# Kernel optimization log

Hardware: AMD Instinct MI355X
Metric: run time of the kernel (lower is better)

The kernel has to match this reference:

```python
import jax, jax.numpy as jnp
import numpy as np

N, K, D = 500000, 16, 16


def setup_inputs() -> dict:
    key = jax.random.key(0)
    k1, k2, k3, k4 = jax.random.split(key, 4)
    x = jax.random.normal(k1, (N, D), dtype=jnp.float32)
    # mixture weights: positive, sum to 1, shape (1, K)
    pi = jax.nn.softmax(jax.random.normal(k2, (1, K), dtype=jnp.float32), axis=-1)
    mu = jax.random.normal(k3, (K, 1, D), dtype=jnp.float32)
    # SPD covariance per cluster: A A^T / D + I
    A = jax.random.normal(k4, (K, D, D), dtype=jnp.float32)
    Sigma = jnp.einsum('kde,kfe->kdf', A, A) / D + jnp.eye(D, dtype=jnp.float32)
    return {"x": x, "pi": pi, "mu": mu, "Sigma": Sigma}


def reference(x, pi, mu, Sigma):
    # Batched MultivariateNormal log_prob over K clusters (replaces the
    # Python loop over torch.distributions.MultivariateNormal).
    d = x.shape[-1]
    L = jnp.linalg.cholesky(Sigma)                      # (K, D, D)
    diff = x[None, :, :] - mu                           # (K, N, D) via mu (K,1,D)
    # solve L y = diff^T per cluster -> Mahalanobis = ||y||^2
    y = jax.vmap(lambda Lk, dk: jax.scipy.linalg.solve_triangular(Lk, dk.T, lower=True))(L, diff)  # (K, D, N)
    maha = jnp.sum(y * y, axis=1)                       # (K, N)
    half_logdet = jnp.sum(jnp.log(jnp.diagonal(L, axis1=-2, axis2=-1)), axis=-1)  # (K,)
    log2pi = jnp.log(jnp.asarray(2.0 * np.pi, dtype=x.dtype))
    logp = -0.5 * (maha + d * log2pi) - half_logdet[:, None]  # (K, N)
    res_k = jnp.exp(logp).T * pi                        # (N, K), pi broadcasts from (1,K)
    res = res_k / jnp.sum(res_k, axis=1, keepdims=True)  # (N, K)
    return res
```

## Files before the change

### kernel.cpp

```cpp
#include <hip/hip_runtime.h>
#include <math.h>

#define D 16
#define K 16
#define BLK 64
#define MPT 2
#define PSTRIDE 176

__host__ __device__ constexpr int tri(int i, int j) { return i * (i + 1) / 2 + j; }

__global__ __launch_bounds__(64) void gmm_prep(
    const float* __restrict__ pi, const float* __restrict__ mu,
    const float* __restrict__ Sigma, float* __restrict__ P)
{
    const int k = threadIdx.x;
    if (k >= K) return;

    float M[tri(D - 1, D - 1) + 1];

#pragma unroll
    for (int i = 0; i < D; ++i)
#pragma unroll
        for (int j = 0; j <= i; ++j)
            M[tri(i, j)] = Sigma[k * D * D + i * D + j];

    float hl = 0.f;
#pragma unroll
    for (int j = 0; j < D; ++j) {
        float s = M[tri(j, j)];
#pragma unroll
        for (int p = 0; p < j; ++p) s -= M[tri(j, p)] * M[tri(j, p)];
        float ljj = sqrtf(s);
        M[tri(j, j)] = ljj;
        hl += logf(ljj);
        float inv = 1.f / ljj;
#pragma unroll
        for (int i = j + 1; i < D; ++i) {
            float t = M[tri(i, j)];
#pragma unroll
            for (int p = 0; p < j; ++p) t -= M[tri(i, p)] * M[tri(j, p)];
            M[tri(i, j)] = t * inv;
        }
    }

#pragma unroll
    for (int j = 0; j < D; ++j) {
        float ujj = 1.f / M[tri(j, j)];
        M[tri(j, j)] = ujj;
#pragma unroll
        for (int i = j + 1; i < D; ++i) {
            float s = 0.f;
#pragma unroll
            for (int p = j; p < i; ++p) s += M[tri(i, p)] * M[tri(p, j)];
            M[tri(i, j)] = -s / M[tri(i, i)];
        }
    }

    const float invs2 = 0.70710678118654752440f;
    float* Pk = P + k * PSTRIDE;
    Pk[0] = logf(pi[k]) - hl;
#pragma unroll
    for (int i = 0; i < D; ++i) {
        float acc = 0.f;
#pragma unroll
        for (int j = 0; j <= i; ++j) acc += M[tri(i, j)] * mu[k * D + j];
        Pk[16 + i] = acc * invs2;
    }
#pragma unroll
    for (int t = 0; t < tri(D - 1, D - 1) + 1; ++t)
        Pk[32 + t] = M[t] * invs2;
}

__global__ __launch_bounds__(BLK) void gmm_main(
    const float* __restrict__ x, const float* __restrict__ P,
    float* __restrict__ out, int N)
{
    const int tid = threadIdx.x;
    const long long base = (long long)blockIdx.x * (BLK * MPT) + tid;

    float xv[MPT][D];
    int   nidx[MPT];
    bool  ok[MPT];
#pragma unroll
    for (int m = 0; m < MPT; ++m) {
        long long n = base + (long long)m * BLK;
        nidx[m] = (int)n;
        ok[m] = (n < (long long)N);
        if (ok[m]) {
            const float4* p = (const float4*)(x + n * D);
            float4 a = p[0], b = p[1], c = p[2], d4 = p[3];
            xv[m][0] = a.x;  xv[m][1] = a.y;  xv[m][2] = a.z;  xv[m][3] = a.w;
            xv[m][4] = b.x;  xv[m][5] = b.y;  xv[m][6] = b.z;  xv[m][7] = b.w;
            xv[m][8] = c.x;  xv[m][9] = c.y;  xv[m][10] = c.z; xv[m][11] = c.w;
            xv[m][12] = d4.x; xv[m][13] = d4.y; xv[m][14] = d4.z; xv[m][15] = d4.w;
        } else {
#pragma unroll
            for (int j = 0; j < D; ++j) xv[m][j] = 0.f;
        }
    }

    float res[MPT][K];
#pragma unroll 1
    for (int k = 0; k < K; ++k) {
        const float* __restrict__ Pk = P + k * PSTRIDE;
        float acc[MPT];
#pragma unroll
        for (int m = 0; m < MPT; ++m) acc[m] = 0.f;
#pragma unroll
        for (int i = 0; i < D; ++i) {
            float tv = Pk[16 + i];
            float y[MPT];
#pragma unroll
            for (int m = 0; m < MPT; ++m) y[m] = -tv;
#pragma unroll
            for (int j = 0; j <= i; ++j) {
                float u = Pk[32 + tri(i, j)];
#pragma unroll
                for (int m = 0; m < MPT; ++m) y[m] = fmaf(u, xv[m][j], y[m]);
            }
#pragma unroll
            for (int m = 0; m < MPT; ++m) acc[m] = fmaf(y[m], y[m], acc[m]);
        }
        float ck = Pk[0];
#pragma unroll
        for (int m = 0; m < MPT; ++m) res[m][k] = ck - acc[m];
    }

#pragma unroll
    for (int m = 0; m < MPT; ++m) {
        if (!ok[m]) continue;
        float mx = res[m][0];
#pragma unroll
        for (int k2 = 1; k2 < K; ++k2) mx = fmaxf(mx, res[m][k2]);
        float sum = 0.f;
#pragma unroll
        for (int k2 = 0; k2 < K; ++k2) {
            float e = __expf(res[m][k2] - mx);
            res[m][k2] = e;
            sum += e;
        }
        float inv = 1.f / sum;
        float4* po = (float4*)(out + (long long)nidx[m] * K);
        float4 o;
        o.x = res[m][0] * inv;  o.y = res[m][1] * inv;
        o.z = res[m][2] * inv;  o.w = res[m][3] * inv;   po[0] = o;
        o.x = res[m][4] * inv;  o.y = res[m][5] * inv;
        o.z = res[m][6] * inv;  o.w = res[m][7] * inv;   po[1] = o;
        o.x = res[m][8] * inv;  o.y = res[m][9] * inv;
        o.z = res[m][10] * inv; o.w = res[m][11] * inv;  po[2] = o;
        o.x = res[m][12] * inv; o.y = res[m][13] * inv;
        o.z = res[m][14] * inv; o.w = res[m][15] * inv;  po[3] = o;
    }
}

extern "C" void kernel_launch(void* const* d_in, const int* in_sizes, int n_in,
                              void* d_out, int out_size, void* d_ws, size_t ws_size,
                              hipStream_t stream) {
    const float* x     = (const float*)d_in[0];
    const float* pi    = (const float*)d_in[1];
    const float* mu    = (const float*)d_in[2];
    const float* Sigma = (const float*)d_in[3];
    float* out = (float*)d_out;
    const int N = in_sizes[0] / D;

    float* P = (float*)d_ws;

    gmm_prep<<<1, 64, 0, stream>>>(pi, mu, Sigma, P);

    const int pts_per_blk = BLK * MPT;
    const int grid = (N + pts_per_blk - 1) / pts_per_blk;
    gmm_main<<<grid, BLK, 0, stream>>>(x, P, out, N);
}
```

Before: 128.7 us.

## Pack Cholesky-inverse rows as fp16 pairs and use dot2 with shared-memory params

```diff
diff --git a/kernel.cpp b/kernel.cpp
--- a/kernel.cpp
+++ b/kernel.cpp
@@ -4,10 +4,32 @@
 #define D 16
 #define K 16
 #define BLK 64
-#define MPT 2
-#define PSTRIDE 176
+#define MPT 4
+#define PK_WORDS 96
+
+typedef _Float16 h2 __attribute__((ext_vector_type(2)));
 
 __host__ __device__ constexpr int tri(int i, int j) { return i * (i + 1) / 2 + j; }
+__host__ __device__ constexpr int rowoff(int i) {
+    int s = 0;
+    for (int r = 0; r < i; ++r) s += (r + 2) / 2;
+    return s;
+}
+
+static __device__ __forceinline__ float fdot2f(h2 a, h2 b, float c) {
+#if __has_builtin(__builtin_amdgcn_fdot2)
+    return __builtin_amdgcn_fdot2(a, b, c, false);
+#else
+    return fmaf((float)a.x, (float)b.x, fmaf((float)a.y, (float)b.y, c));
+#endif
+}
+
+static __device__ __forceinline__ unsigned pack2(float f0, float f1) {
+    _Float16 h0 = (_Float16)f0, h1 = (_Float16)f1;
+    unsigned short b0 = __builtin_bit_cast(unsigned short, h0);
+    unsigned short b1 = __builtin_bit_cast(unsigned short, h1);
+    return ((unsigned)b1 << 16) | (unsigned)b0;
+}
 
 __global__ __launch_bounds__(64) void gmm_prep(
     const float* __restrict__ pi, const float* __restrict__ mu,
@@ -57,99 +79,126 @@
     }
 
     const float invs2 = 0.70710678118654752440f;
-    float* Pk = P + k * PSTRIDE;
+    float* Pk = P + k * PK_WORDS;
+    unsigned* Pu = (unsigned*)Pk;
+
     Pk[0] = logf(pi[k]) - hl;
 #pragma unroll
     for (int i = 0; i < D; ++i) {
         float acc = 0.f;
 #pragma unroll
         for (int j = 0; j <= i; ++j) acc += M[tri(i, j)] * mu[k * D + j];
-        Pk[16 + i] = acc * invs2;
-    }
-#pragma unroll
-    for (int t = 0; t < tri(D - 1, D - 1) + 1; ++t)
-        Pk[32 + t] = M[t] * invs2;
+        Pk[1 + i] = -(acc * invs2);
+    }
+#pragma unroll
+    for (int i = 0; i < D; ++i) {
+        const int np = (i + 2) / 2;
+#pragma unroll
+        for (int p = 0; p < np; ++p) {
+            float f0 = M[tri(i, 2 * p)] * invs2;
+            float f1 = (2 * p + 1 <= i) ? M[tri(i, 2 * p + 1)] * invs2 : 0.f;
+            Pu[17 + rowoff(i) + p] = pack2(f0, f1);
+        }
+    }
+#pragma unroll
+    for (int q = 89; q < PK_WORDS; ++q) Pu[q] = 0;
 }
 
 __global__ __launch_bounds__(BLK) void gmm_main(
     const float* __restrict__ x, const float* __restrict__ P,
     float* __restrict__ out, int N)
 {
+    __shared__ float4 sPv[K * PK_WORDS / 4];
+    __shared__ float  sRes[K][BLK * MPT];
+    float* sP = (float*)sPv;
+
     const int tid = threadIdx.x;
     const long long base = (long long)blockIdx.x * (BLK * MPT) + tid;
 
-    float xv[MPT][D];
-    int   nidx[MPT];
-    bool  ok[MPT];
+    long long n[MPT];
+    bool ok[MPT];
+    float4 xr[MPT][4];
 #pragma unroll
     for (int m = 0; m < MPT; ++m) {
-        long long n = base + (long long)m * BLK;
-        nidx[m] = (int)n;
-        ok[m] = (n < (long long)N);
+        n[m] = base + (long long)m * BLK;
+        ok[m] = (n[m] < (long long)N);
         if (ok[m]) {
-            const float4* p = (const float4*)(x + n * D);
-            float4 a = p[0], b = p[1], c = p[2], d4 = p[3];
-            xv[m][0] = a.x;  xv[m][1] = a.y;  xv[m][2] = a.z;  xv[m][3] = a.w;
-            xv[m][4] = b.x;  xv[m][5] = b.y;  xv[m][6] = b.z;  xv[m][7] = b.w;
-            xv[m][8] = c.x;  xv[m][9] = c.y;  xv[m][10] = c.z; xv[m][11] = c.w;
-            xv[m][12] = d4.x; xv[m][13] = d4.y; xv[m][14] = d4.z; xv[m][15] = d4.w;
+            const float4* p = (const float4*)(x + n[m] * D);
+            xr[m][0] = p[0]; xr[m][1] = p[1]; xr[m][2] = p[2]; xr[m][3] = p[3];
         } else {
-#pragma unroll
-            for (int j = 0; j < D; ++j) xv[m][j] = 0.f;
-        }
-    }
-
-    float res[MPT][K];
+            float4 z = {0, 0, 0, 0};
+            xr[m][0] = z; xr[m][1] = z; xr[m][2] = z; xr[m][3] = z;
+        }
+    }
+
+    const float4* Pv = (const float4*)P;
+    for (int t = tid; t < K * PK_WORDS / 4; t += BLK) sPv[t] = Pv[t];
+    __syncthreads();
+
+    h2 xp[MPT][8];
+#pragma unroll
+    for (int m = 0; m < MPT; ++m)
+#pragma unroll
+        for (int q = 0; q < 4; ++q) {
+            float4 a = xr[m][q];
+            xp[m][2 * q]     = (h2){(_Float16)a.x, (_Float16)a.y};
+            xp[m][2 * q + 1] = (h2){(_Float16)a.z, (_Float16)a.w};
+        }
+
 #pragma unroll 1
     for (int k = 0; k < K; ++k) {
-        const float* __restrict__ Pk = P + k * PSTRIDE;
+        const float* Pk = sP + k * PK_WORDS;
+        const unsigned* Uk = (const unsigned*)(Pk + 17);
         float acc[MPT];
 #pragma unroll
         for (int m = 0; m < MPT; ++m) acc[m] = 0.f;
 #pragma unroll
         for (int i = 0; i < D; ++i) {
-            float tv = Pk[16 + i];
+            const float nt = Pk[1 + i];
             float y[MPT];
 #pragma unroll
-            for (int m = 0; m < MPT; ++m) y[m] = -tv;
-#pragma unroll
-            for (int j = 0; j <= i; ++j) {
-                float u = Pk[32 + tri(i, j)];
-#pragma unroll
-                for (int m = 0; m < MPT; ++m) y[m] = fmaf(u, xv[m][j], y[m]);
+            for (int m = 0; m < MPT; ++m) y[m] = nt;
+            const int np = (i + 2) / 2;
+#pragma unroll
+            for (int p = 0; p < np; ++p) {
+                h2 u = __builtin_bit_cast(h2, Uk[rowoff(i) + p]);
+#pragma unroll
+                for (int m = 0; m < MPT; ++m)
+                    y[m] = fdot2f(u, xp[m][p], y[m]);
             }
 #pragma unroll
             for (int m = 0; m < MPT; ++m) acc[m] = fmaf(y[m], y[m], acc[m]);
         }
-        float ck = Pk[0];
-#pragma unroll
-        for (int m = 0; m < MPT; ++m) res[m][k] = ck - acc[m];
-    }
+        const float ck = Pk[0];
+#pragma unroll
+        for (int m = 0; m < MPT; ++m)
+            sRes[k][m * BLK + tid] = ck - acc[m];
+    }
+    __syncthreads();
 
 #pragma unroll
     for (int m = 0; m < MPT; ++m) {
-        if (!ok[m]) continue;
-        float mx = res[m][0];
-#pragma unroll
-        for (int k2 = 1; k2 < K; ++k2) mx = fmaxf(mx, res[m][k2]);
+        float r[K];
+#pragma unroll
+        for (int k = 0; k < K; ++k) r[k] = sRes[k][m * BLK + tid];
+        float mx = r[0];
+#pragma unroll
+        for (int k = 1; k < K; ++k) mx = fmaxf(mx, r[k]);
         float sum = 0.f;
 #pragma unroll
-        for (int k2 = 0; k2 < K; ++k2) {
-            float e = __expf(res[m][k2] - mx);
-            res[m][k2] = e;
+        for (int k = 0; k < K; ++k) {
+            float e = __expf(r[k] - mx);
+            r[k] = e;
             sum += e;
         }
         float inv = 1.f / sum;
-        float4* po = (float4*)(out + (long long)nidx[m] * K);
-        float4 o;
-        o.x = res[m][0] * inv;  o.y = res[m][1] * inv;
-        o.z = res[m][2] * inv;  o.w = res[m][3] * inv;   po[0] = o;
-        o.x = res[m][4] * inv;  o.y = res[m][5] * inv;
-        o.z = res[m][6] * inv;  o.w = res[m][7] * inv;   po[1] = o;
-        o.x = res[m][8] * inv;  o.y = res[m][9] * inv;
-        o.z = res[m][10] * inv; o.w = res[m][11] * inv;  po[2] = o;
-        o.x = res[m][12] * inv; o.y = res[m][13] * inv;
-        o.z = res[m][14] * inv; o.w = res[m][15] * inv;  po[3] = o;
+        if (ok[m]) {
+            float4* po = (float4*)(out + n[m] * D);
+            po[0] = (float4){r[0] * inv,  r[1] * inv,  r[2] * inv,  r[3] * inv};
+            po[1] = (float4){r[4] * inv,  r[5] * inv,  r[6] * inv,  r[7] * inv};
+            po[2] = (float4){r[8] * inv,  r[9] * inv,  r[10] * inv, r[11] * inv};
+            po[3] = (float4){r[12] * inv, r[13] * inv, r[14] * inv, r[15] * inv};
+        }
     }
 }
 
```

New measurement: 138.4 us. +7.6%, slower.
